# Kernel tuning notes

Measured on AMD Instinct MI355X. Metric: run time of the kernel, lower is better.

The kernel has to match this reference:

```python
import jax, jax.numpy as jnp
import numpy as np

# module constants derived from init kwargs
GROUPS = 4
L_CH = 96    # l_channels = out_channels - int(0.25*out_channels)
NL_CH = 32   # nl_channels


def setup_inputs() -> dict:
    key = jax.random.key(0)
    ks = jax.random.split(key, 10)
    B, C, N, K = 4, 128, 2048, 16
    x = jax.random.normal(ks[0], (B, C, N, K), dtype=jnp.float32)
    abs_x = jax.random.normal(ks[1], (B, C // 2, N, 1), dtype=jnp.float32)
    # distinct kNN-style neighbor indices per point (values in [0, N))
    r = jax.random.uniform(ks[2], (B, 1, N, N))
    idx = jnp.argsort(r, axis=-1)[..., :K].astype(jnp.int32)
    Wq = jax.random.normal(ks[3], (L_CH, C), dtype=jnp.float32) * 0.05
    Wk = jax.random.normal(ks[4], (L_CH, C), dtype=jnp.float32) * 0.05
    Wv = jax.random.normal(ks[5], (L_CH, C), dtype=jnp.float32) * 0.05
    Wnq = jax.random.normal(ks[6], (NL_CH, C // 2), dtype=jnp.float32) * 0.05
    Wnk = jax.random.normal(ks[7], (NL_CH, C // 2), dtype=jnp.float32) * 0.05
    Wnv = jax.random.normal(ks[8], (NL_CH, C // 2), dtype=jnp.float32) * 0.05
    return {"x": x, "abs_x": abs_x, "idx": idx, "Wq": Wq, "Wk": Wk, "Wv": Wv,
            "Wnq": Wnq, "Wnk": Wnk, "Wnv": Wnv}


def reference(x, abs_x, idx, Wq, Wk, Wv, Wnq, Wnk, Wnv):
    B, C, N, K = x.shape
    G = GROUPS
    Clg = L_CH // G   # local channels per group
    Cng = NL_CH // G  # non-local channels per group

    # --- 1. Local attention over K neighbors ---
    # 1x1 conv projections, split into heads: [B, G, Clg, N, K]
    q = jnp.einsum('oc,bcnk->bonk', Wq, x).reshape(B, G, Clg, N, K)
    k = jnp.einsum('oc,bcnk->bonk', Wk, x).reshape(B, G, Clg, N, K)
    v = jnp.einsum('oc,bcnk->bonk', Wv, x).reshape(B, G, Clg, N, K)
    # attention weights over neighbors: [B, G, N, K]
    out = jax.nn.softmax((q * k).sum(axis=2), axis=-1)

    # 1.6 scatter local scores into dense [B, G, N, N] and aggregate per target node
    bi = jnp.arange(B)[:, None, None, None]
    gi = jnp.arange(G)[None, :, None, None]
    ni = jnp.arange(N)[None, None, :, None]
    idx_g = jnp.broadcast_to(idx, (B, G, N, K))  # idx is [B,1,N,K]
    score_mat = jnp.zeros((B, G, N, N), dtype=out.dtype).at[bi, gi, ni, idx_g].set(out)
    score = score_mat.sum(axis=2)                     # [B, G, N]
    val_score, idx_score = jax.lax.top_k(score, K)    # [B, G, K]

    # 1.7 weighted sum of V over neighbors -> [B, G, Clg, N]
    out_l = jnp.einsum('bgnk,bgcnk->bgcn', out, v).reshape(B, L_CH, N, 1)

    # --- 2. Non-local attention over top-K selected nodes ---
    qn = jnp.einsum('oc,bcnk->bonk', Wnq, abs_x).reshape(B, G, Cng, N)
    kn = jnp.einsum('oc,bcnk->bonk', Wnk, abs_x).reshape(B, G, Cng, N)
    vn = jnp.einsum('oc,bcnk->bonk', Wnv, abs_x).reshape(B, G, Cng, N)
    sel = idx_score[:, :, None, :]                    # [B, G, 1, K]
    kn_g = jnp.take_along_axis(kn, jnp.broadcast_to(sel, (B, G, Cng, K)), axis=3)
    vn_g = jnp.take_along_axis(vn, jnp.broadcast_to(sel, (B, G, Cng, K)), axis=3)
    vn_g = vn_g * jnp.tanh(val_score)[:, :, None, :]
    att = jax.nn.softmax(jnp.einsum('bgcn,bgck->bgnk', qn, kn_g), axis=-1)  # [B,G,N,K]
    out_nl = jnp.einsum('bgnk,bgck->bgcn', att, vn_g).reshape(B, NL_CH, N, 1)

    # --- 3. Concat (layer > 0) ---
    return jnp.concatenate([out_l, out_nl], axis=1)  # [B, out_channels, N, 1]
```

## Files before the change

### kernel.cpp

```cpp
#include <hip/hip_runtime.h>
#include <math.h>

#define B   4
#define C   128
#define N   2048
#define K   16
#define G   4
#define LCH 96
#define NLCH 32
#define CLG 24
#define CNG 8
#define CH  64
#define NT  16
#define CPAD (C + 4)

__global__ __launch_bounds__(512, 3) void k_local(
    const float* __restrict__ x, const int* __restrict__ idx,
    const float* __restrict__ Wq, const float* __restrict__ Wk,
    const float* __restrict__ Wv,
    float* __restrict__ out, float* __restrict__ score)
{
    __shared__ float ps[G][2][NT][K];
    __shared__ float yls[G][NT][CPAD];

    const int blk = blockIdx.x;
    const int b  = blk >> 7;
    const int n0 = (blk & 127) << 4;
    const int tid  = threadIdx.x;
    const int lane = tid & 63;
    const int wid = __builtin_amdgcn_readfirstlane(tid >> 6);
    const int g = wid >> 1, h = wid & 1;
    const int kk = lane >> 2, m = lane & 3;

    const float4* wq4 = reinterpret_cast<const float4*>(Wq + (size_t)(g * CLG + h * 12) * C);
    const float4* wk4 = reinterpret_cast<const float4*>(Wk + (size_t)(g * CLG + h * 12) * C);

    const float* xb = x + ((size_t)b * C * N + (size_t)n0) * K + m * K + kk;

    float accq[12][4], acck[12][4];
#pragma unroll
    for (int i = 0; i < 12; i++)
#pragma unroll
        for (int j = 0; j < 4; j++) { accq[i][j] = 0.f; acck[i][j] = 0.f; }

    for (int c4 = 0; c4 < C / 4; c4++) {
        float xv[4][4];
#pragma unroll
        for (int cc = 0; cc < 4; cc++) {
            const float* p = xb + (size_t)(c4 * 4 + cc) * (N * K);
#pragma unroll
            for (int j = 0; j < 4; j++) xv[cc][j] = p[j * 64];
        }
#pragma unroll
        for (int i = 0; i < 12; i++) {
            const float4 aq = wq4[i * (C / 4) + c4];
            const float4 ak = wk4[i * (C / 4) + c4];
#pragma unroll
            for (int j = 0; j < 4; j++) {
                accq[i][j] = fmaf(aq.x, xv[0][j], accq[i][j]);
                accq[i][j] = fmaf(aq.y, xv[1][j], accq[i][j]);
                accq[i][j] = fmaf(aq.z, xv[2][j], accq[i][j]);
                accq[i][j] = fmaf(aq.w, xv[3][j], accq[i][j]);
                acck[i][j] = fmaf(ak.x, xv[0][j], acck[i][j]);
                acck[i][j] = fmaf(ak.y, xv[1][j], acck[i][j]);
                acck[i][j] = fmaf(ak.z, xv[2][j], acck[i][j]);
                acck[i][j] = fmaf(ak.w, xv[3][j], acck[i][j]);
            }
        }
    }

#pragma unroll
    for (int j = 0; j < 4; j++) {
        float s = 0.f;
#pragma unroll
        for (int i = 0; i < 12; i++) s = fmaf(accq[i][j], acck[i][j], s);
        ps[g][h][m + 4 * j][kk] = s;
    }
    __syncthreads();

    float ow[4];
#pragma unroll
    for (int j = 0; j < 4; j++) {
        float s = ps[g][0][m + 4 * j][kk] + ps[g][1][m + 4 * j][kk];
        float mx = s;
        mx = fmaxf(mx, __shfl_xor(mx, 4));
        mx = fmaxf(mx, __shfl_xor(mx, 8));
        mx = fmaxf(mx, __shfl_xor(mx, 16));
        mx = fmaxf(mx, __shfl_xor(mx, 32));
        const float e = expf(s - mx);
        float sum = e;
        sum += __shfl_xor(sum, 4);
        sum += __shfl_xor(sum, 8);
        sum += __shfl_xor(sum, 16);
        sum += __shfl_xor(sum, 32);
        ow[j] = e / sum;
    }

    if (h == 0) {
#pragma unroll
        for (int j = 0; j < 4; j++) {
            const int mi = idx[((size_t)b * N + n0 + m + 4 * j) * K + kk];
            atomicAdd(&score[(b * G + g) * N + mi], ow[j]);
        }
    }

    for (int c = h * 64; c < h * 64 + 64; c++) {
        const float* p = xb + (size_t)c * (N * K);
        float t0 = ow[0] * p[0];
        float t1 = ow[1] * p[64];
        float t2 = ow[2] * p[128];
        float t3 = ow[3] * p[192];
        t0 += __shfl_xor(t0, 4); t0 += __shfl_xor(t0, 8); t0 += __shfl_xor(t0, 16); t0 += __shfl_xor(t0, 32);
        t1 += __shfl_xor(t1, 4); t1 += __shfl_xor(t1, 8); t1 += __shfl_xor(t1, 16); t1 += __shfl_xor(t1, 32);
        t2 += __shfl_xor(t2, 4); t2 += __shfl_xor(t2, 8); t2 += __shfl_xor(t2, 16); t2 += __shfl_xor(t2, 32);
        t3 += __shfl_xor(t3, 4); t3 += __shfl_xor(t3, 8); t3 += __shfl_xor(t3, 16); t3 += __shfl_xor(t3, 32);
        if (kk == 0) {
            yls[g][m + 0][c]  = t0;
            yls[g][m + 4][c]  = t1;
            yls[g][m + 8][c]  = t2;
            yls[g][m + 12][c] = t3;
        }
    }
    __syncthreads();

#pragma unroll
    for (int rep = 0; rep < 3; rep++) {
        const int o = rep * 32 + (tid >> 4);
        const int n = tid & 15;
        const float4* wv4 = reinterpret_cast<const float4*>(Wv + (size_t)o * C);
        const float* yr = &yls[o / CLG][n][0];
        float acc = 0.f;
        for (int c4 = 0; c4 < C / 4; c4++) {
            const float4 wv = wv4[c4];
            const float4 yv = *reinterpret_cast<const float4*>(&yr[c4 * 4]);
            acc = fmaf(wv.x, yv.x, fmaf(wv.y, yv.y, fmaf(wv.z, yv.z, fmaf(wv.w, yv.w, acc))));
        }
        out[((size_t)b * C + o) * N + n0 + n] = acc;
    }
}

__global__ __launch_bounds__(256) void k_topk(
    const float* __restrict__ abs_x, const float* __restrict__ score,
    const float* __restrict__ Wnk, const float* __restrict__ Wnv,
    float* __restrict__ kng, float* __restrict__ vng)
{
    __shared__ float s[N];
    __shared__ float rv[4];
    __shared__ int   ri[4];
    __shared__ int   selS[K];
    __shared__ float valS[K];
    __shared__ float axs[CH][K];

    const int bg = blockIdx.x;
    const int b = bg >> 2, g = bg & 3;
    const int tid = threadIdx.x;
    const int lane = tid & 63, w = tid >> 6;

    for (int i = tid; i < N; i += 256) s[i] = score[bg * N + i];
    __syncthreads();

    for (int t = 0; t < K; t++) {
        float bv = -INFINITY; int bi = N;
        for (int i = tid; i < N; i += 256) {
            const float v = s[i];
            if (v > bv) { bv = v; bi = i; }
        }
#pragma unroll
        for (int mask = 1; mask < 64; mask <<= 1) {
            const float ov = __shfl_xor(bv, mask);
            const int   oi = __shfl_xor(bi, mask);
            if (ov > bv || (ov == bv && oi < bi)) { bv = ov; bi = oi; }
        }
        if (lane == 0) { rv[w] = bv; ri[w] = bi; }
        __syncthreads();
        if (tid == 0) {
            float fv = rv[0]; int fi = ri[0];
            for (int j = 1; j < 4; j++)
                if (rv[j] > fv || (rv[j] == fv && ri[j] < fi)) { fv = rv[j]; fi = ri[j]; }
            selS[t] = fi; valS[t] = fv; s[fi] = -INFINITY;
        }
        __syncthreads();
    }

    for (int i = tid; i < CH * K; i += 256) {
        const int cc = i >> 4, kk = i & 15;
        axs[cc][kk] = abs_x[((size_t)b * CH + cc) * N + selS[kk]];
    }
    __syncthreads();

    {
        const int c = tid >> 5, kk = (tid >> 1) & 15, hh = tid & 1;
        const float* wkr = Wnk + ((size_t)g * CNG + c) * CH + hh * 32;
        const float* wvr = Wnv + ((size_t)g * CNG + c) * CH + hh * 32;
        float ka = 0.f, va = 0.f;
#pragma unroll 8
        for (int cc = 0; cc < 32; cc++) {
            const float ax = axs[hh * 32 + cc][kk];
            ka = fmaf(wkr[cc], ax, ka);
            va = fmaf(wvr[cc], ax, va);
        }
        ka += __shfl_xor(ka, 1);
        va += __shfl_xor(va, 1);
        if (hh == 0) {
            va *= tanhf(valS[kk]);
            kng[bg * CNG * K + c * K + kk] = ka;
            vng[bg * CNG * K + c * K + kk] = va;
        }
    }
}

__global__ __launch_bounds__(64) void k_nonlocal(
    const float* __restrict__ abs_x, const float* __restrict__ Wnq,
    const float* __restrict__ kng, const float* __restrict__ vng,
    float* __restrict__ out)
{
    __shared__ float skn[CNG * K];
    __shared__ float svn[CNG * K];

    const int blk = blockIdx.x;
    const int b = blk >> 7;
    const int g = (blk >> 5) & 3;
    const int n = ((blk & 31) << 6) + threadIdx.x;
    const int bg = b * G + g;

    for (int i = threadIdx.x; i < CNG * K; i += 64) {
        skn[i] = kng[bg * CNG * K + i];
        svn[i] = vng[bg * CNG * K + i];
    }
    __syncthreads();

    float qn[CNG];
#pragma unroll
    for (int c = 0; c < CNG; c++) qn[c] = 0.f;
    const float* wqn = Wnq + (size_t)g * CNG * CH;
#pragma unroll 4
    for (int cc = 0; cc < CH; cc++) {
        const float ax = abs_x[((size_t)b * CH + cc) * N + n];
#pragma unroll
        for (int c = 0; c < CNG; c++)
            qn[c] = fmaf(wqn[c * CH + cc], ax, qn[c]);
    }

    float sc[K];
#pragma unroll
    for (int kk = 0; kk < K; kk++) {
        float v = 0.f;
#pragma unroll
        for (int c = 0; c < CNG; c++) v = fmaf(qn[c], skn[c * K + kk], v);
        sc[kk] = v;
    }
    float m = sc[0];
#pragma unroll
    for (int kk = 1; kk < K; kk++) m = fmaxf(m, sc[kk]);
    float sum = 0.f;
#pragma unroll
    for (int kk = 0; kk < K; kk++) { sc[kk] = expf(sc[kk] - m); sum += sc[kk]; }
    const float inv = 1.f / sum;
#pragma unroll
    for (int c = 0; c < CNG; c++) {
        float acc = 0.f;
#pragma unroll
        for (int kk = 0; kk < K; kk++)
            acc = fmaf(sc[kk] * inv, svn[c * K + kk], acc);
        out[((size_t)b * C + LCH + g * CNG + c) * N + n] = acc;
    }
}

extern "C" void kernel_launch(void* const* d_in, const int* in_sizes, int n_in,
                              void* d_out, int out_size, void* d_ws, size_t ws_size,
                              hipStream_t stream) {
    const float* x     = (const float*)d_in[0];
    const float* abs_x = (const float*)d_in[1];
    const int*   idx   = (const int*)d_in[2];
    const float* Wq    = (const float*)d_in[3];
    const float* Wk    = (const float*)d_in[4];
    const float* Wv    = (const float*)d_in[5];
    const float* Wnq   = (const float*)d_in[6];
    const float* Wnk   = (const float*)d_in[7];
    const float* Wnv   = (const float*)d_in[8];
    float* out = (float*)d_out;

    float* ws    = (float*)d_ws;
    float* score = ws;
    float* kng   = ws + B * G * N;
    float* vng   = kng + B * G * CNG * K;

    hipMemsetAsync(score, 0, (size_t)B * G * N * sizeof(float), stream);

    k_local<<<B * (N / NT), 512, 0, stream>>>(x, idx, Wq, Wk, Wv, out, score);
    k_topk<<<B * G, 256, 0, stream>>>(abs_x, score, Wnk, Wnv, kng, vng);
    k_nonlocal<<<B * G * N / 64, 64, 0, stream>>>(abs_x, Wnq, kng, vng, out);
}
```

Measured before the change: 290.9 us.

## Halve local-attention node tile and software-prefetch next x channel slice

Cuts the local-attention block tile from 16 to 8 nodes, which doubles the grid to 1024 blocks and halves per-thread accumulator registers. It also adds a register double buffer that loads the next four channels of x while the current ones are used in FMAs. The Wv projection epilogue is remapped to 8 nodes with a guard on output channels. In exchange, weight loads are amortized over fewer nodes and launch bounds drop to 2 blocks per SM.

```diff
diff --git a/kernel.cpp b/kernel.cpp
--- a/kernel.cpp
+++ b/kernel.cpp
@@ -11,10 +11,10 @@
 #define CLG 24
 #define CNG 8
 #define CH  64
-#define NT  16
+#define NT  8
 #define CPAD (C + 4)
 
-__global__ __launch_bounds__(512, 3) void k_local(
+__global__ __launch_bounds__(512, 2) void k_local(
     const float* __restrict__ x, const int* __restrict__ idx,
     const float* __restrict__ Wq, const float* __restrict__ Wk,
     const float* __restrict__ Wv,
@@ -24,8 +24,8 @@
     __shared__ float yls[G][NT][CPAD];
 
     const int blk = blockIdx.x;
-    const int b  = blk >> 7;
-    const int n0 = (blk & 127) << 4;
+    const int b  = blk >> 8;
+    const int n0 = (blk & 255) << 3;
     const int tid  = threadIdx.x;
     const int lane = tid & 63;
     const int wid = __builtin_amdgcn_readfirstlane(tid >> 6);
@@ -37,40 +37,52 @@
 
     const float* xb = x + ((size_t)b * C * N + (size_t)n0) * K + m * K + kk;
 
-    float accq[12][4], acck[12][4];
+    float accq[12][2], acck[12][2];
 #pragma unroll
     for (int i = 0; i < 12; i++)
 #pragma unroll
-        for (int j = 0; j < 4; j++) { accq[i][j] = 0.f; acck[i][j] = 0.f; }
+        for (int j = 0; j < 2; j++) { accq[i][j] = 0.f; acck[i][j] = 0.f; }
+
+    float cur[4][2], nxt[4][2];
+#pragma unroll
+    for (int cc = 0; cc < 4; cc++)
+#pragma unroll
+        for (int j = 0; j < 2; j++)
+            cur[cc][j] = xb[(size_t)cc * (N * K) + j * 64];
 
     for (int c4 = 0; c4 < C / 4; c4++) {
-        float xv[4][4];
-#pragma unroll
-        for (int cc = 0; cc < 4; cc++) {
-            const float* p = xb + (size_t)(c4 * 4 + cc) * (N * K);
-#pragma unroll
-            for (int j = 0; j < 4; j++) xv[cc][j] = p[j * 64];
+        if (c4 < C / 4 - 1) {
+#pragma unroll
+            for (int cc = 0; cc < 4; cc++)
+#pragma unroll
+                for (int j = 0; j < 2; j++)
+                    nxt[cc][j] = xb[(size_t)((c4 + 1) * 4 + cc) * (N * K) + j * 64];
         }
 #pragma unroll
         for (int i = 0; i < 12; i++) {
             const float4 aq = wq4[i * (C / 4) + c4];
             const float4 ak = wk4[i * (C / 4) + c4];
 #pragma unroll
-            for (int j = 0; j < 4; j++) {
-                accq[i][j] = fmaf(aq.x, xv[0][j], accq[i][j]);
-                accq[i][j] = fmaf(aq.y, xv[1][j], accq[i][j]);
-                accq[i][j] = fmaf(aq.z, xv[2][j], accq[i][j]);
-                accq[i][j] = fmaf(aq.w, xv[3][j], accq[i][j]);
-                acck[i][j] = fmaf(ak.x, xv[0][j], acck[i][j]);
-                acck[i][j] = fmaf(ak.y, xv[1][j], acck[i][j]);
-                acck[i][j] = fmaf(ak.z, xv[2][j], acck[i][j]);
-                acck[i][j] = fmaf(ak.w, xv[3][j], acck[i][j]);
+            for (int j = 0; j < 2; j++) {
+                accq[i][j] = fmaf(aq.x, cur[0][j], accq[i][j]);
+                accq[i][j] = fmaf(aq.y, cur[1][j], accq[i][j]);
+                accq[i][j] = fmaf(aq.z, cur[2][j], accq[i][j]);
+                accq[i][j] = fmaf(aq.w, cur[3][j], accq[i][j]);
+                acck[i][j] = fmaf(ak.x, cur[0][j], acck[i][j]);
+                acck[i][j] = fmaf(ak.y, cur[1][j], acck[i][j]);
+                acck[i][j] = fmaf(ak.z, cur[2][j], acck[i][j]);
+                acck[i][j] = fmaf(ak.w, cur[3][j], acck[i][j]);
             }
         }
-    }
-
-#pragma unroll
-    for (int j = 0; j < 4; j++) {
+#pragma unroll
+        for (int cc = 0; cc < 4; cc++)
+#pragma unroll
+            for (int j = 0; j < 2; j++)
+                cur[cc][j] = nxt[cc][j];
+    }
+
+#pragma unroll
+    for (int j = 0; j < 2; j++) {
         float s = 0.f;
 #pragma unroll
         for (int i = 0; i < 12; i++) s = fmaf(accq[i][j], acck[i][j], s);
@@ -78,9 +90,9 @@
     }
     __syncthreads();
 
-    float ow[4];
-#pragma unroll
-    for (int j = 0; j < 4; j++) {
+    float ow[2];
+#pragma unroll
+    for (int j = 0; j < 2; j++) {
         float s = ps[g][0][m + 4 * j][kk] + ps[g][1][m + 4 * j][kk];
         float mx = s;
         mx = fmaxf(mx, __shfl_xor(mx, 4));
@@ -98,7 +110,7 @@
 
     if (h == 0) {
 #pragma unroll
-        for (int j = 0; j < 4; j++) {
+        for (int j = 0; j < 2; j++) {
             const int mi = idx[((size_t)b * N + n0 + m + 4 * j) * K + kk];
             atomicAdd(&score[(b * G + g) * N + mi], ow[j]);
         }
@@ -108,34 +120,30 @@
         const float* p = xb + (size_t)c * (N * K);
         float t0 = ow[0] * p[0];
         float t1 = ow[1] * p[64];
-        float t2 = ow[2] * p[128];
-        float t3 = ow[3] * p[192];
         t0 += __shfl_xor(t0, 4); t0 += __shfl_xor(t0, 8); t0 += __shfl_xor(t0, 16); t0 += __shfl_xor(t0, 32);
         t1 += __shfl_xor(t1, 4); t1 += __shfl_xor(t1, 8); t1 += __shfl_xor(t1, 16); t1 += __shfl_xor(t1, 32);
-        t2 += __shfl_xor(t2, 4); t2 += __shfl_xor(t2, 8); t2 += __shfl_xor(t2, 16); t2 += __shfl_xor(t2, 32);
-        t3 += __shfl_xor(t3, 4); t3 += __shfl_xor(t3, 8); t3 += __shfl_xor(t3, 16); t3 += __shfl_xor(t3, 32);
         if (kk == 0) {
-            yls[g][m + 0][c]  = t0;
-            yls[g][m + 4][c]  = t1;
-            yls[g][m + 8][c]  = t2;
-            yls[g][m + 12][c] = t3;
-        }
-    }
-    __syncthreads();
-
-#pragma unroll
-    for (int rep = 0; rep < 3; rep++) {
-        const int o = rep * 32 + (tid >> 4);
-        const int n = tid & 15;
-        const float4* wv4 = reinterpret_cast<const float4*>(Wv + (size_t)o * C);
-        const float* yr = &yls[o / CLG][n][0];
-        float acc = 0.f;
-        for (int c4 = 0; c4 < C / 4; c4++) {
-            const float4 wv = wv4[c4];
-            const float4 yv = *reinterpret_cast<const float4*>(&yr[c4 * 4]);
-            acc = fmaf(wv.x, yv.x, fmaf(wv.y, yv.y, fmaf(wv.z, yv.z, fmaf(wv.w, yv.w, acc))));
-        }
-        out[((size_t)b * C + o) * N + n0 + n] = acc;
+            yls[g][m][c]     = t0;
+            yls[g][m + 4][c] = t1;
+        }
+    }
+    __syncthreads();
+
+#pragma unroll
+    for (int rep = 0; rep < 2; rep++) {
+        const int o = rep * 64 + (tid >> 3);
+        const int n = tid & 7;
+        if (o < LCH) {
+            const float4* wv4 = reinterpret_cast<const float4*>(Wv + (size_t)o * C);
+            const float* yr = &yls[o / CLG][n][0];
+            float acc = 0.f;
+            for (int c4 = 0; c4 < C / 4; c4++) {
+                const float4 wv = wv4[c4];
+                const float4 yv = *reinterpret_cast<const float4*>(&yr[c4 * 4]);
+                acc = fmaf(wv.x, yv.x, fmaf(wv.y, yv.y, fmaf(wv.z, yv.z, fmaf(wv.w, yv.w, acc))));
+            }
+            out[((size_t)b * C + o) * N + n0 + n] = acc;
+        }
     }
 }
 
```

Measured after the change: 264.8 us. -9.0%, faster.
